# Optimization experiments

Hardware: AMD Instinct MI355X
Metric: run time of the kernel (lower is better)

## Reference

```python
import jax, jax.numpy as jnp
import numpy as np

RADIUS = 0.8
NSAMPLE = 32
EPS = 1e-5  # BatchNorm eps


def _bn(x, gamma, beta, axes):
    # BatchNorm (training-mode batch statistics), channel dim kept via broadcasting
    m = jnp.mean(x, axis=axes, keepdims=True)
    v = jnp.var(x, axis=axes, keepdims=True)
    return (x - m) * jax.lax.rsqrt(v + EPS) * gamma + beta


def setup_inputs() -> dict:
    key = jax.random.key(0)
    ks = jax.random.split(key, 6)
    B, N, P, C, COUT = 4, 8192, 2048, 128, 256
    ffps_xyz = jax.random.uniform(ks[0], (B, P, 3), dtype=jnp.float32) * 2.0 - 1.0
    backbone_xyz = jax.random.uniform(ks[1], (B, N, 3), dtype=jnp.float32) * 2.0 - 1.0
    backbone_features = jax.random.normal(ks[2], (B, C, N), dtype=jnp.float32)
    w_shift = jax.random.normal(ks[3], (3, 3), dtype=jnp.float32) * 0.1
    gamma_shift = jnp.ones((3,), jnp.float32)
    beta_shift = jnp.zeros((3,), jnp.float32)
    w_mlp = jax.random.normal(ks[4], (COUT, 3 + C), dtype=jnp.float32) * 0.05
    gamma_mlp = jnp.ones((COUT,), jnp.float32)
    beta_mlp = jnp.zeros((COUT,), jnp.float32)
    return {
        "ffps_xyz": ffps_xyz,
        "backbone_xyz": backbone_xyz,
        "backbone_features": backbone_features,
        "w_shift": w_shift,
        "gamma_shift": gamma_shift,
        "beta_shift": beta_shift,
        "w_mlp": w_mlp,
        "gamma_mlp": gamma_mlp,
        "beta_mlp": beta_mlp,
    }


def reference(ffps_xyz, backbone_xyz, backbone_features,
              w_shift, gamma_shift, beta_shift,
              w_mlp, gamma_mlp, beta_mlp):
    B, P, _ = ffps_xyz.shape
    N = backbone_xyz.shape[1]

    # ---- shift_layer: Conv1d(3->3, k=1, no bias) + BN1d + ReLU on (B,3,P) ----
    x = jnp.einsum('oc,bpc->bop', w_shift, ffps_xyz)                  # (B,3,P)
    x = _bn(x, gamma_shift[None, :, None], beta_shift[None, :, None], (0, 2))
    new_xyz = jax.nn.relu(x).transpose(0, 2, 1)                       # (B,P,3) query centers

    # ---- QueryAndGroup: ball query (radius, nsample), use_xyz=True ----
    d2 = jnp.sum((new_xyz[:, :, None, :] - backbone_xyz[:, None, :, :]) ** 2, -1)  # (B,P,N)
    within = d2 < (RADIUS * RADIUS)
    # pick the first NSAMPLE in-radius indices (CUDA ball_query semantics)
    keyv = jnp.where(within, jnp.arange(N, dtype=jnp.int32), jnp.int32(N))
    negk, idx = jax.lax.top_k(-keyv, NSAMPLE)                          # smallest keys first
    valid = (-negk) < N
    idx = jnp.where(valid, idx, idx[..., :1])                          # pad with first found idx

    g_xyz = jnp.take_along_axis(backbone_xyz[:, None, :, :], idx[..., None], axis=2)
    g_xyz = g_xyz - new_xyz[:, :, None, :]                             # (B,P,S,3) recentered
    feats = backbone_features.transpose(0, 2, 1)                       # (B,N,C)
    g_f = jnp.take_along_axis(feats[:, None, :, :], idx[..., None], axis=2)  # (B,P,S,C)
    g = jnp.concatenate([g_xyz, g_f], axis=-1)                         # (B,P,S,3+C)

    # ---- mlp: 1x1 conv (3+C -> COUT, no bias) + BN + ReLU ----
    y = jnp.einsum('oc,bpsc->bops', w_mlp, g)                          # (B,COUT,P,S)
    y = _bn(y, gamma_mlp[None, :, None, None], beta_mlp[None, :, None, None], (0, 2, 3))
    y = jax.nn.relu(y)

    # ---- max-pool over neighbor axis, squeeze, transpose ----
    y = jnp.max(y, axis=3)                                             # (B,COUT,P)
    return y.transpose(0, 2, 1)                                        # (B,P,COUT)
```

## Files before the change

### kernel.cpp

```cpp
#include <hip/hip_runtime.h>
#include <math.h>

namespace {
constexpr int B    = 4;
constexpr int N    = 8192;
constexpr int P    = 2048;
constexpr int C    = 128;
constexpr int COUT = 256;
constexpr int NS   = 32;
constexpr int BP   = B * P;
constexpr int BPB  = 2;
constexpr int GRP  = 8;
constexpr int NBLK = (BP / (BPB * GRP)) * 2;

constexpr size_t OFF_FEATT = 0;
constexpr size_t OFF_WSWZ  = 8388608;
constexpr size_t OFF_SSLOT = 8470528;
constexpr size_t OFF_SUMS  = 8471040;
constexpr size_t OFF_IDX   = 8475136;
constexpr size_t OFF_GX    = 9523712;
constexpr size_t OFF_YMAX  = 11620864;
constexpr size_t WS_NEED   = 20009472;
}

typedef short bf16x8 __attribute__((ext_vector_type(8)));
typedef float f32x4  __attribute__((ext_vector_type(4)));

typedef const __attribute__((address_space(1))) void gas_void;
typedef __attribute__((address_space(3))) void las_void;
#define GLOBAL_LOAD_LDS16(gp, lp) \
    __builtin_amdgcn_global_load_lds((gas_void*)(gp), (las_void*)(lp), 16, 0, 0)

__device__ inline unsigned short f2bf(float f) {
    unsigned u = __float_as_uint(f);
    unsigned r = u + 0x7fffu + ((u >> 16) & 1u);
    return (unsigned short)(r >> 16);
}


__global__ __launch_bounds__(256) void k_prep(const float* __restrict__ ffps,
                                              const float* __restrict__ wsh,
                                              double* __restrict__ sslot,
                                              float* __restrict__ sums) {
#pragma clang fp contract(off)
    int blk = blockIdx.x, t = threadIdx.x;
    if (blk == 8) {
        ((f32x4*)sums)[t & 127] = (f32x4){0.f, 0.f, 0.f, 0.f};
        return;
    }
    __shared__ double red[6][256];
    double w[9];
#pragma unroll
    for (int i = 0; i < 9; i++) w[i] = (double)wsh[i];
    double s[3] = {0, 0, 0}, sq[3] = {0, 0, 0};
#pragma unroll
    for (int i = 0; i < 4; i++) {
        int p = blk * 1024 + t + 256 * i;
        double f0 = (double)ffps[p * 3 + 0];
        double f1 = (double)ffps[p * 3 + 1];
        double f2 = (double)ffps[p * 3 + 2];
#pragma unroll
        for (int o = 0; o < 3; o++) {
            double xo = (w[o * 3 + 0] * f0 + w[o * 3 + 1] * f1) + w[o * 3 + 2] * f2;
            s[o] += xo;
            sq[o] += xo * xo;
        }
    }
#pragma unroll
    for (int o = 0; o < 3; o++) { red[o][t] = s[o]; red[3 + o][t] = sq[o]; }
    for (int off = 128; off > 0; off >>= 1) {
        __syncthreads();
        if (t < off) {
#pragma unroll
            for (int j = 0; j < 6; j++) red[j][t] += red[j][t + off];
        }
    }
    __syncthreads();
    if (t < 6) sslot[blk * 6 + t] = red[t][0];
}

__global__ __launch_bounds__(256) void k_front(const float* __restrict__ ffps,
                                               const float* __restrict__ bbxyz,
                                               const float* __restrict__ feat,
                                               const float* __restrict__ wsh,
                                               const float* __restrict__ gsh,
                                               const float* __restrict__ bsh,
                                               const float* __restrict__ wml,
                                               const double* __restrict__ sslot,
                                               unsigned short* __restrict__ featT,
                                               unsigned short* __restrict__ wswz,
                                               int* __restrict__ idxo,
                                               uint2* __restrict__ gxo) {
#pragma clang fp contract(off)
    int blk = blockIdx.x, t = threadIdx.x;
    if (blk >= 2048) {
        int rb = blk - 2048;
        if (rb < 2048) {
            __shared__ float tile[64][33];
            int tx = t & 31, ty = t >> 5;
            int n0 = (rb & 255) * 32, c0 = ((rb >> 8) & 1) * 64, b = rb >> 9;
            const float* src = feat + ((size_t)b * C + c0) * N + n0;
#pragma unroll
            for (int j = 0; j < 8; j++) tile[ty + 8 * j][tx] = src[(size_t)(ty + 8 * j) * N + tx];
            __syncthreads();
            int n = t >> 3;
            int k8 = (t & 7) * 8;
            unsigned vv[4];
#pragma unroll
            for (int i = 0; i < 4; i++) {
                unsigned lo = f2bf(tile[k8 + 2 * i][n]);
                unsigned hi = f2bf(tile[k8 + 2 * i + 1][n]);
                vv[i] = lo | (hi << 16);
            }
            *(int4*)&featT[((size_t)b * N + n0 + n) * C + c0 + k8] =
                make_int4((int)vv[0], (int)vv[1], (int)vv[2], (int)vv[3]);
        } else {
            int i = (rb - 2048) * 256 + t;
            int j = i & 7;
            int lane = (i >> 3) & 63;
            int rest = i >> 9;
            int ks = rest % 5, rt = rest / 5;
            int cout = rt * 16 + (lane & 15);
            int k = ks * 32 + (lane >> 4) * 8 + j;
            float v = 0.f;
            if (k < 128) v = wml[cout * 131 + 3 + k];
            else if (k < 131) v = wml[cout * 131 + (k - 128)];
            wswz[i] = f2bf(v);
        }
        return;
    }

    __shared__ double spar[6];
    if (t < 6) {
        double a = 0.0;
        for (int r = 0; r < 8; r++) a += sslot[r * 6 + t];
        spar[t] = a;
    }
    __syncthreads();
    int wv = t >> 6, lane = t & 63;
    int q = blk * 4 + wv;
    int b = q >> 11;
    double f0 = (double)ffps[q * 3 + 0];
    double f1 = (double)ffps[q * 3 + 1];
    double f2 = (double)ffps[q * 3 + 2];
    double qd[3];
#pragma unroll
    for (int o = 0; o < 3; o++) {
        double m  = spar[o] * (1.0 / 8192.0);
        double v  = spar[3 + o] * (1.0 / 8192.0) - m * m;
        double is = 1.0 / sqrt(v + 1e-5);
        double x  = ((double)wsh[o * 3 + 0] * f0 + (double)wsh[o * 3 + 1] * f1) +
                    (double)wsh[o * 3 + 2] * f2;
        double y  = ((x - m) * is) * (double)gsh[o] + (double)bsh[o];
        qd[o] = (y > 0.0) ? y : 0.0;
    }
    double qx = qd[0], qy = qd[1], qz = qd[2];
    float cfx = (float)qx, cfy = (float)qy, cfz = (float)qz;
    const float* base = bbxyz + (size_t)b * N * 3;
    const double R2 = 0.8 * 0.8;
    const float R2F = 0.64f;
    {
        double ex = fmax(fmax(qx - 1.0, -1.0 - qx), 0.0);
        double ey = fmax(fmax(qy - 1.0, -1.0 - qy), 0.0);
        double ez = fmax(fmax(qz - 1.0, -1.0 - qz), 0.0);
        if (ex * ex + ey * ey + ez * ez >= R2) {
            if (lane < NS) {
                idxo[q * NS + lane] = 0;
                float rx = base[0] - cfx, ry = base[1] - cfy, rz = base[2] - cfz;
                unsigned u01 = (unsigned)f2bf(rx) | ((unsigned)f2bf(ry) << 16);
                gxo[q * NS + lane] = make_uint2(u01, (unsigned)f2bf(rz));
            }
            return;
        }
    }
    int found = 0, firstn = -1;

    float X0[8], Y0[8], Z0[8], X1[8], Y1[8], Z1[8];

    auto loadb = [&](float (&XX)[8], float (&YY)[8], float (&ZZ)[8], int it) {
#pragma unroll
        for (int j = 0; j < 8; j++) {
            int n = it * 512 + j * 64 + lane;
            XX[j] = base[n * 3 + 0];
            YY[j] = base[n * 3 + 1];
            ZZ[j] = base[n * 3 + 2];
        }
    };
    auto proc = [&](float (&XX)[8], float (&YY)[8], float (&ZZ)[8], int it) {
#pragma clang fp contract(off)
#pragma unroll
        for (int j = 0; j < 8; j++) {
            int n = it * 512 + j * 64 + lane;
            float dxf = cfx - XX[j];
            float dyf = cfy - YY[j];
            float dzf = cfz - ZZ[j];
            float d2f = (dxf * dxf + dyf * dyf) + dzf * dzf;
            bool within;
            if (__builtin_expect(fabsf(d2f - R2F) < 1e-4f, 0)) {
                double dx = qx - (double)XX[j];
                double dy = qy - (double)YY[j];
                double dz = qz - (double)ZZ[j];
                within = ((dx * dx + dy * dy) + dz * dz) < R2;
            } else {
                within = d2f < R2F;
            }
            unsigned long long mask = __ballot(within);
            if (firstn < 0 && mask != 0ull) firstn = (n - lane) + (__ffsll(mask) - 1);
            if (within) {
                int rank = found + __popcll(mask & ((1ull << lane) - 1ull));
                if (rank < NS) {
                    idxo[q * NS + rank] = n;
                    float rx = XX[j] - cfx, ry = YY[j] - cfy, rz = ZZ[j] - cfz;
                    unsigned u01 = (unsigned)f2bf(rx) | ((unsigned)f2bf(ry) << 16);
                    gxo[q * NS + rank] = make_uint2(u01, (unsigned)f2bf(rz));
                }
            }
            found += __popcll(mask);
        }
    };

    loadb(X0, Y0, Z0, 0);
    loadb(X1, Y1, Z1, 1);

    for (int it = 0; it < 16; it += 2) {
        proc(X0, Y0, Z0, it);
        if (found >= NS) break;
        loadb(X0, Y0, Z0, (it + 2 < 16) ? it + 2 : 0);
        if (it + 1 >= 16) break;
        proc(X1, Y1, Z1, it + 1);
        if (found >= NS) break;
        loadb(X1, Y1, Z1, (it + 3 < 16) ? it + 3 : 0);
    }
    if (found < NS) {
        int padv = (found == 0) ? 0 : firstn;
        if (lane >= found && lane < NS) {
            idxo[q * NS + lane] = padv;
            float rx = base[padv * 3 + 0] - cfx;
            float ry = base[padv * 3 + 1] - cfy;
            float rz = base[padv * 3 + 2] - cfz;
            unsigned u01 = (unsigned)f2bf(rx) | ((unsigned)f2bf(ry) << 16);
            gxo[q * NS + lane] = make_uint2(u01, (unsigned)f2bf(rz));
        }
    }
}

__global__ __launch_bounds__(256, 3) void k_mlp_mfma(
        const unsigned short* __restrict__ featT,
        const unsigned short* __restrict__ wswz,
        const int* __restrict__ idx,
        const uint2* __restrict__ gxyz,
        float* __restrict__ ymax,
        float* __restrict__ sums) {
    __shared__ alignas(16) unsigned short G[2][4 * 4 * 64 * 8];
    int t = threadIdx.x, lane = t & 63, w = t >> 6;
    int q = lane >> 4, c16 = lane & 15;
    int d = blockIdx.x;
    int blk = ((d & 7) >> 1) * 256 + (d >> 3) * 2 + (d & 1);
    int nh = blk & 1;
    int bpbase = (blk >> 1) * (BPB * GRP);
    const bf16x8* wp = (const bf16x8*)wswz;

    bf16x8 wreg[5][2];
#pragma unroll
    for (int ks = 0; ks < 5; ks++)
#pragma unroll
        for (int nt = 0; nt < 2; nt++)
            wreg[ks][nt] = wp[((nh * 8 + w * 2 + nt) * 5 + ks) * 64 + lane];

    int sOff = (w >> 1) * NS + (w & 1) * 16 + c16;
    size_t fb = (size_t)(bpbase >> 11) * N * C;

    int nS0 = idx[bpbase * NS + sOff] & (N - 1);
    int nS1 = idx[(bpbase + BPB) * NS + sOff] & (N - 1);
    uint2 gx_c[4] = {}, gx_n[4] = {};
    if (q == 0)
#pragma unroll
        for (int mt = 0; mt < 4; mt++)
            gx_c[mt] = gxyz[(bpbase + (mt >> 1)) * NS + (mt & 1) * 16 + c16];
    {
        const unsigned short* row = featT + fb + (size_t)nS0 * C + q * 8;
#pragma unroll
        for (int ks = 0; ks < 4; ks++)
            GLOBAL_LOAD_LDS16(row + ks * 32, &G[0][(w * 4 + ks) * 512]);
    }

    float smA[2] = {0.f, 0.f}, sqA[2] = {0.f, 0.f};

    for (int g = 0; g < GRP; g++) {
        int buf = g & 1;
        int bp0 = bpbase + g * BPB;
        __syncthreads();
        if (g + 1 < GRP) {
            const unsigned short* row = featT + fb + (size_t)nS1 * C + q * 8;
#pragma unroll
            for (int ks = 0; ks < 4; ks++)
                GLOBAL_LOAD_LDS16(row + ks * 32, &G[buf ^ 1][(w * 4 + ks) * 512]);
            if (q == 0)
#pragma unroll
                for (int mt = 0; mt < 4; mt++)
                    gx_n[mt] = gxyz[(bp0 + BPB + (mt >> 1)) * NS + (mt & 1) * 16 + c16];
        }
        if (g + 2 < GRP) nS0 = idx[(bp0 + 2 * BPB) * NS + sOff] & (N - 1);

        f32x4 acc[4][2];
#pragma unroll
        for (int mt = 0; mt < 4; mt++)
#pragma unroll
            for (int nt = 0; nt < 2; nt++) acc[mt][nt] = (f32x4){0.f, 0.f, 0.f, 0.f};

#pragma unroll
        for (int ks = 0; ks < 4; ks++) {
            bf16x8 ag[4];
#pragma unroll
            for (int mt = 0; mt < 4; mt++)
                ag[mt] = *(const bf16x8*)&G[buf][((mt * 4 + ks) * 64 + lane) * 8];
#pragma unroll
            for (int nt = 0; nt < 2; nt++)
#pragma unroll
                for (int mt = 0; mt < 4; mt++)
                    acc[mt][nt] = __builtin_amdgcn_mfma_f32_16x16x32_bf16(ag[mt], wreg[ks][nt], acc[mt][nt], 0, 0, 0);
        }
        {
            bf16x8 agx[4];
#pragma unroll
            for (int mt = 0; mt < 4; mt++) {
                union { int4 i; bf16x8 h; } u;
                u.i = make_int4(q == 0 ? (int)gx_c[mt].x : 0,
                                q == 0 ? (int)gx_c[mt].y : 0, 0, 0);
                agx[mt] = u.h;
            }
#pragma unroll
            for (int nt = 0; nt < 2; nt++)
#pragma unroll
                for (int mt = 0; mt < 4; mt++)
                    acc[mt][nt] = __builtin_amdgcn_mfma_f32_16x16x32_bf16(agx[mt], wreg[4][nt], acc[mt][nt], 0, 0, 0);
        }

#pragma unroll
        for (int pm = 0; pm < BPB; pm++) {
            int bp = bp0 + pm;
#pragma unroll
            for (int nt = 0; nt < 2; nt++) {
                f32x4 a = acc[2 * pm][nt], c = acc[2 * pm + 1][nt];
                float mx = fmaxf(fmaxf(fmaxf(a[0], a[1]), fmaxf(a[2], a[3])),
                                 fmaxf(fmaxf(c[0], c[1]), fmaxf(c[2], c[3])));
                smA[nt] += ((a[0] + a[1]) + (a[2] + a[3])) + ((c[0] + c[1]) + (c[2] + c[3]));
                sqA[nt] += ((a[0] * a[0] + a[1] * a[1]) + (a[2] * a[2] + a[3] * a[3])) +
                           ((c[0] * c[0] + c[1] * c[1]) + (c[2] * c[2] + c[3] * c[3]));
                mx = fmaxf(mx, __shfl_xor(mx, 16, 64));
                mx = fmaxf(mx, __shfl_xor(mx, 32, 64));
                if (q == 0)
                    ymax[(size_t)bp * COUT + nh * 128 + w * 32 + nt * 16 + c16] = mx;
            }
        }
        nS1 = nS0;
#pragma unroll
        for (int mt = 0; mt < 4; mt++) gx_c[mt] = gx_n[mt];
    }

#pragma unroll
    for (int nt = 0; nt < 2; nt++) {
        float sm = smA[nt], sq = sqA[nt];
        sm += __shfl_xor(sm, 16, 64);
        sm += __shfl_xor(sm, 32, 64);
        sq += __shfl_xor(sq, 16, 64);
        sq += __shfl_xor(sq, 32, 64);
        if (q == 0) {
            int cout = nh * 128 + w * 32 + nt * 16 + c16;
            atomicAdd(&sums[cout], sm);
            atomicAdd(&sums[256 + cout], sq);
        }
    }
}

__global__ __launch_bounds__(256) void k_final(const float* __restrict__ ymax,
                                               const float* __restrict__ sums,
                                               const float* __restrict__ gam,
                                               const float* __restrict__ bet,
                                               float* __restrict__ out) {
    __shared__ float sa[256], sb[256];
    int t = threadIdx.x;
    {
        double sm = (double)sums[t], sq = (double)sums[256 + t];
        double mean = sm * (1.0 / 262144.0);
        double var = sq * (1.0 / 262144.0) - mean * mean;
        double a = (double)gam[t] / sqrt(var + 1e-5);
        sa[t] = (float)a;
        sb[t] = (float)((double)bet[t] - mean * a);
    }
    __syncthreads();
    int i = blockIdx.x * 256 + t;
    int c0 = (t & 63) * 4;
    f32x4 y = *(const f32x4*)&ymax[(size_t)i * 4];
    f32x4 r;
#pragma unroll
    for (int j = 0; j < 4; j++) r[j] = fmaxf(sa[c0 + j] * y[j] + sb[c0 + j], 0.f);
    *(f32x4*)&out[(size_t)i * 4] = r;
}

extern "C" void kernel_launch(void* const* d_in, const int* in_sizes, int n_in,
                              void* d_out, int out_size, void* d_ws, size_t ws_size,
                              hipStream_t stream) {
    const float* ffps  = (const float*)d_in[0];
    const float* bbxyz = (const float*)d_in[1];
    const float* feat  = (const float*)d_in[2];
    const float* wsh   = (const float*)d_in[3];
    const float* gsh   = (const float*)d_in[4];
    const float* bsh   = (const float*)d_in[5];
    const float* wml   = (const float*)d_in[6];
    const float* gml   = (const float*)d_in[7];
    const float* bml   = (const float*)d_in[8];
    float* out = (float*)d_out;
    char* ws = (char*)d_ws;
    if (ws_size < WS_NEED) return;

    unsigned short* featT = (unsigned short*)(ws + OFF_FEATT);
    unsigned short* wswz  = (unsigned short*)(ws + OFF_WSWZ);
    double*         sslot = (double*)(ws + OFF_SSLOT);
    float*          sums  = (float*)(ws + OFF_SUMS);
    int*            idx   = (int*)(ws + OFF_IDX);
    uint2*          gx    = (uint2*)(ws + OFF_GX);
    float*          ymax  = (float*)(ws + OFF_YMAX);

    k_prep<<<dim3(9), dim3(256), 0, stream>>>(ffps, wsh, sslot, sums);
    k_front<<<dim3(2048 + 2048 + 160), dim3(256), 0, stream>>>(
        ffps, bbxyz, feat, wsh, gsh, bsh, wml, sslot, featT, wswz, idx, gx);
    k_mlp_mfma<<<dim3(NBLK), dim3(256), 0, stream>>>(featT, wswz, idx, gx, ymax, sums);
    k_final<<<dim3(BP * COUT / 1024), dim3(256), 0, stream>>>(ymax, sums, gml, bml, out);
}
```

Before: 152.0 us.

## Fuse MLP and BN finalize into a cooperative kernel with grid sync

Replaces the separate MLP kernel and final BN/ReLU kernel with one cooperative kernel. Each block covers all 256 output channels for 16 query points, keeps the per-point max in shared memory, and after a grid-wide sync applies the BN scale/shift and writes the output directly. This removes the round trip of the ymax buffer through global memory and one kernel launch. In exchange it uses more registers per block, halves the block count, and relies on all 512 blocks being co-resident; if the cooperative launch fails it falls back to the old two-kernel path.

```diff
diff --git a/kernel.cpp b/kernel.cpp
--- a/kernel.cpp
+++ b/kernel.cpp
@@ -1,5 +1,8 @@
 #include <hip/hip_runtime.h>
+#include <hip/hip_cooperative_groups.h>
 #include <math.h>
+
+namespace cg = cooperative_groups;
 
 namespace {
 constexpr int B    = 4;
@@ -11,7 +14,8 @@
 constexpr int BP   = B * P;
 constexpr int BPB  = 2;
 constexpr int GRP  = 8;
-constexpr int NBLK = (BP / (BPB * GRP)) * 2;
+constexpr int NBLKC = BP / (BPB * GRP);
+constexpr int NBLKL = NBLKC * 2;
 
 constexpr size_t OFF_FEATT = 0;
 constexpr size_t OFF_WSWZ  = 8388608;
@@ -244,6 +248,155 @@
     }
 }
 
+__global__ __launch_bounds__(256, 2) void k_mlp_coop(
+        const unsigned short* __restrict__ featT,
+        const unsigned short* __restrict__ wswz,
+        const int* __restrict__ idx,
+        const uint2* __restrict__ gxyz,
+        const float* __restrict__ gam,
+        const float* __restrict__ bet,
+        float* __restrict__ sums,
+        float* __restrict__ out) {
+    cg::grid_group grid = cg::this_grid();
+    __shared__ alignas(16) unsigned short G[2][4 * 4 * 64 * 8];
+    __shared__ float ymx[16][COUT];
+    __shared__ float sa[COUT], sb[COUT];
+    int t = threadIdx.x, lane = t & 63, w = t >> 6;
+    int q = lane >> 4, c16 = lane & 15;
+    int d = blockIdx.x;
+    int blk = ((d & 7) >> 1) * 128 + (d >> 3) * 2 + (d & 1);
+    int bpbase = blk * (BPB * GRP);
+    const bf16x8* wp = (const bf16x8*)wswz;
+
+    bf16x8 wreg[5][4];
+#pragma unroll
+    for (int ks = 0; ks < 5; ks++)
+#pragma unroll
+        for (int nt = 0; nt < 4; nt++)
+            wreg[ks][nt] = wp[((w * 4 + nt) * 5 + ks) * 64 + lane];
+
+    int sOff = (w >> 1) * NS + (w & 1) * 16 + c16;
+    size_t fb = (size_t)(bpbase >> 11) * N * C;
+
+    int nS0 = idx[bpbase * NS + sOff] & (N - 1);
+    int nS1 = idx[(bpbase + BPB) * NS + sOff] & (N - 1);
+    uint2 gx_c[4] = {}, gx_n[4] = {};
+    if (q == 0)
+#pragma unroll
+        for (int mt = 0; mt < 4; mt++)
+            gx_c[mt] = gxyz[(bpbase + (mt >> 1)) * NS + (mt & 1) * 16 + c16];
+    {
+        const unsigned short* row = featT + fb + (size_t)nS0 * C + q * 8;
+#pragma unroll
+        for (int ks = 0; ks < 4; ks++)
+            GLOBAL_LOAD_LDS16(row + ks * 32, &G[0][(w * 4 + ks) * 512]);
+    }
+
+    float smA[4] = {0.f, 0.f, 0.f, 0.f}, sqA[4] = {0.f, 0.f, 0.f, 0.f};
+
+    for (int g = 0; g < GRP; g++) {
+        int buf = g & 1;
+        int bp0l = g * BPB;
+        __syncthreads();
+        if (g + 1 < GRP) {
+            const unsigned short* row = featT + fb + (size_t)nS1 * C + q * 8;
+#pragma unroll
+            for (int ks = 0; ks < 4; ks++)
+                GLOBAL_LOAD_LDS16(row + ks * 32, &G[buf ^ 1][(w * 4 + ks) * 512]);
+            if (q == 0)
+#pragma unroll
+                for (int mt = 0; mt < 4; mt++)
+                    gx_n[mt] = gxyz[(bpbase + bp0l + BPB + (mt >> 1)) * NS + (mt & 1) * 16 + c16];
+        }
+        if (g + 2 < GRP) nS0 = idx[(bpbase + bp0l + 2 * BPB) * NS + sOff] & (N - 1);
+
+        f32x4 acc[4][4];
+#pragma unroll
+        for (int mt = 0; mt < 4; mt++)
+#pragma unroll
+            for (int nt = 0; nt < 4; nt++) acc[mt][nt] = (f32x4){0.f, 0.f, 0.f, 0.f};
+
+#pragma unroll
+        for (int ks = 0; ks < 4; ks++) {
+            bf16x8 ag[4];
+#pragma unroll
+            for (int mt = 0; mt < 4; mt++)
+                ag[mt] = *(const bf16x8*)&G[buf][((mt * 4 + ks) * 64 + lane) * 8];
+#pragma unroll
+            for (int nt = 0; nt < 4; nt++)
+#pragma unroll
+                for (int mt = 0; mt < 4; mt++)
+                    acc[mt][nt] = __builtin_amdgcn_mfma_f32_16x16x32_bf16(ag[mt], wreg[ks][nt], acc[mt][nt], 0, 0, 0);
+        }
+        {
+            bf16x8 agx[4];
+#pragma unroll
+            for (int mt = 0; mt < 4; mt++) {
+                union { int4 i; bf16x8 h; } u;
+                u.i = make_int4(q == 0 ? (int)gx_c[mt].x : 0,
+                                q == 0 ? (int)gx_c[mt].y : 0, 0, 0);
+                agx[mt] = u.h;
+            }
+#pragma unroll
+            for (int nt = 0; nt < 4; nt++)
+#pragma unroll
+                for (int mt = 0; mt < 4; mt++)
+                    acc[mt][nt] = __builtin_amdgcn_mfma_f32_16x16x32_bf16(agx[mt], wreg[4][nt], acc[mt][nt], 0, 0, 0);
+        }
+
+#pragma unroll
+        for (int pm = 0; pm < BPB; pm++) {
+#pragma unroll
+            for (int nt = 0; nt < 4; nt++) {
+                f32x4 a = acc[2 * pm][nt], c = acc[2 * pm + 1][nt];
+                float mx = fmaxf(fmaxf(fmaxf(a[0], a[1]), fmaxf(a[2], a[3])),
+                                 fmaxf(fmaxf(c[0], c[1]), fmaxf(c[2], c[3])));
+                smA[nt] += ((a[0] + a[1]) + (a[2] + a[3])) + ((c[0] + c[1]) + (c[2] + c[3]));
+                sqA[nt] += ((a[0] * a[0] + a[1] * a[1]) + (a[2] * a[2] + a[3] * a[3])) +
+                           ((c[0] * c[0] + c[1] * c[1]) + (c[2] * c[2] + c[3] * c[3]));
+                mx = fmaxf(mx, __shfl_xor(mx, 16, 64));
+                mx = fmaxf(mx, __shfl_xor(mx, 32, 64));
+                if (q == 0)
+                    ymx[bp0l + pm][w * 64 + nt * 16 + c16] = mx;
+            }
+        }
+        nS1 = nS0;
+#pragma unroll
+        for (int mt = 0; mt < 4; mt++) gx_c[mt] = gx_n[mt];
+    }
+
+#pragma unroll
+    for (int nt = 0; nt < 4; nt++) {
+        float sm = smA[nt], sq = sqA[nt];
+        sm += __shfl_xor(sm, 16, 64);
+        sm += __shfl_xor(sm, 32, 64);
+        sq += __shfl_xor(sq, 16, 64);
+        sq += __shfl_xor(sq, 32, 64);
+        if (q == 0) {
+            int cout = w * 64 + nt * 16 + c16;
+            atomicAdd(&sums[cout], sm);
+            atomicAdd(&sums[256 + cout], sq);
+        }
+    }
+
+    grid.sync();
+
+    {
+        float smv = __hip_atomic_load(&sums[t], __ATOMIC_RELAXED, __HIP_MEMORY_SCOPE_AGENT);
+        float sqv = __hip_atomic_load(&sums[256 + t], __ATOMIC_RELAXED, __HIP_MEMORY_SCOPE_AGENT);
+        double mean = (double)smv * (1.0 / 262144.0);
+        double var  = (double)sqv * (1.0 / 262144.0) - mean * mean;
+        double a = (double)gam[t] / sqrt(var + 1e-5);
+        sa[t] = (float)a;
+        sb[t] = (float)((double)bet[t] - mean * a);
+    }
+    __syncthreads();
+    for (int r = 0; r < 16; r++) {
+        float y = ymx[r][t];
+        out[(size_t)(bpbase + r) * COUT + t] = fmaxf(sa[t] * y + sb[t], 0.f);
+    }
+}
+
 __global__ __launch_bounds__(256, 3) void k_mlp_mfma(
         const unsigned short* __restrict__ featT,
         const unsigned short* __restrict__ wswz,
@@ -259,17 +412,14 @@
     int nh = blk & 1;
     int bpbase = (blk >> 1) * (BPB * GRP);
     const bf16x8* wp = (const bf16x8*)wswz;
-
     bf16x8 wreg[5][2];
 #pragma unroll
     for (int ks = 0; ks < 5; ks++)
 #pragma unroll
         for (int nt = 0; nt < 2; nt++)
             wreg[ks][nt] = wp[((nh * 8 + w * 2 + nt) * 5 + ks) * 64 + lane];
-
     int sOff = (w >> 1) * NS + (w & 1) * 16 + c16;
     size_t fb = (size_t)(bpbase >> 11) * N * C;
-
     int nS0 = idx[bpbase * NS + sOff] & (N - 1);
     int nS1 = idx[(bpbase + BPB) * NS + sOff] & (N - 1);
     uint2 gx_c[4] = {}, gx_n[4] = {};
@@ -283,9 +433,7 @@
         for (int ks = 0; ks < 4; ks++)
             GLOBAL_LOAD_LDS16(row + ks * 32, &G[0][(w * 4 + ks) * 512]);
     }
-
     float smA[2] = {0.f, 0.f}, sqA[2] = {0.f, 0.f};
-
     for (int g = 0; g < GRP; g++) {
         int buf = g & 1;
         int bp0 = bpbase + g * BPB;
@@ -301,13 +449,11 @@
                     gx_n[mt] = gxyz[(bp0 + BPB + (mt >> 1)) * NS + (mt & 1) * 16 + c16];
         }
         if (g + 2 < GRP) nS0 = idx[(bp0 + 2 * BPB) * NS + sOff] & (N - 1);
-
         f32x4 acc[4][2];
 #pragma unroll
         for (int mt = 0; mt < 4; mt++)
 #pragma unroll
             for (int nt = 0; nt < 2; nt++) acc[mt][nt] = (f32x4){0.f, 0.f, 0.f, 0.f};
-
 #pragma unroll
         for (int ks = 0; ks < 4; ks++) {
             bf16x8 ag[4];
@@ -335,7 +481,6 @@
                 for (int mt = 0; mt < 4; mt++)
                     acc[mt][nt] = __builtin_amdgcn_mfma_f32_16x16x32_bf16(agx[mt], wreg[4][nt], acc[mt][nt], 0, 0, 0);
         }
-
 #pragma unroll
         for (int pm = 0; pm < BPB; pm++) {
             int bp = bp0 + pm;
@@ -357,7 +502,6 @@
 #pragma unroll
         for (int mt = 0; mt < 4; mt++) gx_c[mt] = gx_n[mt];
     }
-
 #pragma unroll
     for (int nt = 0; nt < 2; nt++) {
         float sm = smA[nt], sq = sqA[nt];
@@ -425,6 +569,13 @@
     k_prep<<<dim3(9), dim3(256), 0, stream>>>(ffps, wsh, sslot, sums);
     k_front<<<dim3(2048 + 2048 + 160), dim3(256), 0, stream>>>(
         ffps, bbxyz, feat, wsh, gsh, bsh, wml, sslot, featT, wswz, idx, gx);
-    k_mlp_mfma<<<dim3(NBLK), dim3(256), 0, stream>>>(featT, wswz, idx, gx, ymax, sums);
-    k_final<<<dim3(BP * COUT / 1024), dim3(256), 0, stream>>>(ymax, sums, gml, bml, out);
-}
+
+    void* kargs[] = {(void*)&featT, (void*)&wswz, (void*)&idx, (void*)&gx,
+                     (void*)&gml, (void*)&bml, (void*)&sums, (void*)&out};
+    hipError_t err = hipLaunchCooperativeKernel((const void*)k_mlp_coop, dim3(NBLKC),
+                                                dim3(256), kargs, 0, stream);
+    if (err != hipSuccess) {
+        k_mlp_mfma<<<dim3(NBLKL), dim3(256), 0, stream>>>(featT, wswz, idx, gx, ymax, sums);
+        k_final<<<dim3(BP * COUT / 1024), dim3(256), 0, stream>>>(ymax, sums, gml, bml, out);
+    }
+}
```

Measured after the change: 222.5 us. +46.4%, slower.

## Split ball-query scan across two waves per query with LDS merge

Applied to the files above, without the earlier changes.

Each query is now handled by two wavefronts that scan the two halves of the point cloud in parallel. Candidates go to shared memory and are merged into the first-32 ordering afterwards, and the second-half wave exits early once the first half has already found 32 neighbours. This shortens the serial scan latency for queries with few in-radius points at the cost of twice the blocks, extra LDS traffic and a block-wide sync. Padding semantics are preserved by choosing the first found index from whichever half has hits.

```diff
diff --git a/kernel.cpp b/kernel.cpp
--- a/kernel.cpp
+++ b/kernel.cpp
@@ -93,8 +93,8 @@
                                                uint2* __restrict__ gxo) {
 #pragma clang fp contract(off)
     int blk = blockIdx.x, t = threadIdx.x;
-    if (blk >= 2048) {
-        int rb = blk - 2048;
+    if (blk >= 4096) {
+        int rb = blk - 4096;
         if (rb < 2048) {
             __shared__ float tile[64][33];
             int tx = t & 31, ty = t >> 5;
@@ -131,14 +131,20 @@
     }
 
     __shared__ double spar[6];
+    __shared__ int lidx[2][2][NS];
+    __shared__ uint2 lgx[2][2][NS];
+    __shared__ int lcnt[2][2], lfirst[2][2];
+    __shared__ int ldone[2];
     if (t < 6) {
         double a = 0.0;
         for (int r = 0; r < 8; r++) a += sslot[r * 6 + t];
         spar[t] = a;
     }
+    if (t < 2) ldone[t] = 0;
     __syncthreads();
     int wv = t >> 6, lane = t & 63;
-    int q = blk * 4 + wv;
+    int qi = wv >> 1, half = wv & 1;
+    int q = blk * 2 + qi;
     int b = q >> 11;
     double f0 = (double)ffps[q * 3 + 0];
     double f1 = (double)ffps[q * 3 + 1];
@@ -159,88 +165,121 @@
     const float* base = bbxyz + (size_t)b * N * 3;
     const double R2 = 0.8 * 0.8;
     const float R2F = 0.64f;
+    bool eo;
     {
         double ex = fmax(fmax(qx - 1.0, -1.0 - qx), 0.0);
         double ey = fmax(fmax(qy - 1.0, -1.0 - qy), 0.0);
         double ez = fmax(fmax(qz - 1.0, -1.0 - qz), 0.0);
-        if (ex * ex + ey * ey + ez * ez >= R2) {
-            if (lane < NS) {
-                idxo[q * NS + lane] = 0;
-                float rx = base[0] - cfx, ry = base[1] - cfy, rz = base[2] - cfz;
-                unsigned u01 = (unsigned)f2bf(rx) | ((unsigned)f2bf(ry) << 16);
-                gxo[q * NS + lane] = make_uint2(u01, (unsigned)f2bf(rz));
+        eo = (ex * ex + ey * ey + ez * ez >= R2);
+    }
+
+    if (!eo) {
+        int found = 0, firstn = -1;
+        int nb = half * 4096;
+
+        float X0[8], Y0[8], Z0[8], X1[8], Y1[8], Z1[8];
+
+        auto loadb = [&](float (&XX)[8], float (&YY)[8], float (&ZZ)[8], int it) {
+#pragma unroll
+            for (int j = 0; j < 8; j++) {
+                int n = nb + it * 512 + j * 64 + lane;
+                XX[j] = base[n * 3 + 0];
+                YY[j] = base[n * 3 + 1];
+                ZZ[j] = base[n * 3 + 2];
             }
-            return;
-        }
-    }
-    int found = 0, firstn = -1;
-
-    float X0[8], Y0[8], Z0[8], X1[8], Y1[8], Z1[8];
-
-    auto loadb = [&](float (&XX)[8], float (&YY)[8], float (&ZZ)[8], int it) {
-#pragma unroll
-        for (int j = 0; j < 8; j++) {
-            int n = it * 512 + j * 64 + lane;
-            XX[j] = base[n * 3 + 0];
-            YY[j] = base[n * 3 + 1];
-            ZZ[j] = base[n * 3 + 2];
-        }
-    };
-    auto proc = [&](float (&XX)[8], float (&YY)[8], float (&ZZ)[8], int it) {
+        };
+        auto proc = [&](float (&XX)[8], float (&YY)[8], float (&ZZ)[8], int it) {
 #pragma clang fp contract(off)
 #pragma unroll
-        for (int j = 0; j < 8; j++) {
-            int n = it * 512 + j * 64 + lane;
-            float dxf = cfx - XX[j];
-            float dyf = cfy - YY[j];
-            float dzf = cfz - ZZ[j];
-            float d2f = (dxf * dxf + dyf * dyf) + dzf * dzf;
-            bool within;
-            if (__builtin_expect(fabsf(d2f - R2F) < 1e-4f, 0)) {
-                double dx = qx - (double)XX[j];
-                double dy = qy - (double)YY[j];
-                double dz = qz - (double)ZZ[j];
-                within = ((dx * dx + dy * dy) + dz * dz) < R2;
-            } else {
-                within = d2f < R2F;
+            for (int j = 0; j < 8; j++) {
+                int n = nb + it * 512 + j * 64 + lane;
+                float dxf = cfx - XX[j];
+                float dyf = cfy - YY[j];
+                float dzf = cfz - ZZ[j];
+                float d2f = (dxf * dxf + dyf * dyf) + dzf * dzf;
+                bool within;
+                if (__builtin_expect(fabsf(d2f - R2F) < 1e-4f, 0)) {
+                    double dx = qx - (double)XX[j];
+                    double dy = qy - (double)YY[j];
+                    double dz = qz - (double)ZZ[j];
+                    within = ((dx * dx + dy * dy) + dz * dz) < R2;
+                } else {
+                    within = d2f < R2F;
+                }
+                unsigned long long mask = __ballot(within);
+                if (firstn < 0 && mask != 0ull) firstn = (n - lane) + (__ffsll(mask) - 1);
+                if (within) {
+                    int rank = found + __popcll(mask & ((1ull << lane) - 1ull));
+                    if (rank < NS) {
+                        lidx[qi][half][rank] = n;
+                        float rx = XX[j] - cfx, ry = YY[j] - cfy, rz = ZZ[j] - cfz;
+                        unsigned u01 = (unsigned)f2bf(rx) | ((unsigned)f2bf(ry) << 16);
+                        lgx[qi][half][rank] = make_uint2(u01, (unsigned)f2bf(rz));
+                    }
+                }
+                found += __popcll(mask);
             }
-            unsigned long long mask = __ballot(within);
-            if (firstn < 0 && mask != 0ull) firstn = (n - lane) + (__ffsll(mask) - 1);
-            if (within) {
-                int rank = found + __popcll(mask & ((1ull << lane) - 1ull));
-                if (rank < NS) {
-                    idxo[q * NS + rank] = n;
-                    float rx = XX[j] - cfx, ry = YY[j] - cfy, rz = ZZ[j] - cfz;
-                    unsigned u01 = (unsigned)f2bf(rx) | ((unsigned)f2bf(ry) << 16);
-                    gxo[q * NS + rank] = make_uint2(u01, (unsigned)f2bf(rz));
-                }
-            }
-            found += __popcll(mask);
-        }
-    };
-
-    loadb(X0, Y0, Z0, 0);
-    loadb(X1, Y1, Z1, 1);
-
-    for (int it = 0; it < 16; it += 2) {
-        proc(X0, Y0, Z0, it);
-        if (found >= NS) break;
-        loadb(X0, Y0, Z0, (it + 2 < 16) ? it + 2 : 0);
-        if (it + 1 >= 16) break;
-        proc(X1, Y1, Z1, it + 1);
-        if (found >= NS) break;
-        loadb(X1, Y1, Z1, (it + 3 < 16) ? it + 3 : 0);
-    }
-    if (found < NS) {
-        int padv = (found == 0) ? 0 : firstn;
-        if (lane >= found && lane < NS) {
-            idxo[q * NS + lane] = padv;
-            float rx = base[padv * 3 + 0] - cfx;
-            float ry = base[padv * 3 + 1] - cfy;
-            float rz = base[padv * 3 + 2] - cfz;
+        };
+
+        loadb(X0, Y0, Z0, 0);
+        loadb(X1, Y1, Z1, 1);
+
+        for (int it = 0; it < 8; it += 2) {
+            proc(X0, Y0, Z0, it);
+            if (found >= NS) break;
+            if (half == 1 &&
+                __hip_atomic_load(&ldone[qi], __ATOMIC_RELAXED, __HIP_MEMORY_SCOPE_WORKGROUP))
+                break;
+            loadb(X0, Y0, Z0, (it + 2 < 8) ? it + 2 : 0);
+            if (it + 1 >= 8) break;
+            proc(X1, Y1, Z1, it + 1);
+            if (found >= NS) break;
+            if (half == 1 &&
+                __hip_atomic_load(&ldone[qi], __ATOMIC_RELAXED, __HIP_MEMORY_SCOPE_WORKGROUP))
+                break;
+            loadb(X1, Y1, Z1, (it + 3 < 8) ? it + 3 : 0);
+        }
+        if (half == 0 && found >= NS)
+            __hip_atomic_store(&ldone[qi], 1, __ATOMIC_RELAXED, __HIP_MEMORY_SCOPE_WORKGROUP);
+        if (lane == 0) {
+            lcnt[qi][half] = found;
+            lfirst[qi][half] = firstn;
+        }
+    }
+    __syncthreads();
+
+    if (eo) {
+        if (half == 0 && lane < NS) {
+            idxo[q * NS + lane] = 0;
+            float rx = base[0] - cfx, ry = base[1] - cfy, rz = base[2] - cfz;
             unsigned u01 = (unsigned)f2bf(rx) | ((unsigned)f2bf(ry) << 16);
             gxo[q * NS + lane] = make_uint2(u01, (unsigned)f2bf(rz));
         }
+    } else if (half == 0 && lane < NS) {
+        int fa = lcnt[qi][0], fb = lcnt[qi][1];
+        int ka = (fa < NS) ? fa : NS;
+        int tot = fa + fb;
+        int kt = (tot < NS) ? tot : NS;
+        int idxv;
+        uint2 gxv;
+        if (lane < ka) {
+            idxv = lidx[qi][0][lane];
+            gxv  = lgx[qi][0][lane];
+        } else if (lane < kt) {
+            idxv = lidx[qi][1][lane - ka];
+            gxv  = lgx[qi][1][lane - ka];
+        } else if (tot > 0) {
+            int hsel = (fa > 0) ? 0 : 1;
+            idxv = lidx[qi][hsel][0];
+            gxv  = lgx[qi][hsel][0];
+        } else {
+            idxv = 0;
+            float rx = base[0] - cfx, ry = base[1] - cfy, rz = base[2] - cfz;
+            unsigned u01 = (unsigned)f2bf(rx) | ((unsigned)f2bf(ry) << 16);
+            gxv = make_uint2(u01, (unsigned)f2bf(rz));
+        }
+        idxo[q * NS + lane] = idxv;
+        gxo[q * NS + lane] = gxv;
     }
 }
 
@@ -423,7 +462,7 @@
     float*          ymax  = (float*)(ws + OFF_YMAX);
 
     k_prep<<<dim3(9), dim3(256), 0, stream>>>(ffps, wsh, sslot, sums);
-    k_front<<<dim3(2048 + 2048 + 160), dim3(256), 0, stream>>>(
+    k_front<<<dim3(4096 + 2048 + 160), dim3(256), 0, stream>>>(
         ffps, bbxyz, feat, wsh, gsh, bsh, wml, sslot, featT, wswz, idx, gx);
     k_mlp_mfma<<<dim3(NBLK), dim3(256), 0, stream>>>(featT, wswz, idx, gx, ymax, sums);
     k_final<<<dim3(BP * COUT / 1024), dim3(256), 0, stream>>>(ymax, sums, gml, bml, out);
```

Result: faster. 148.3 us (median of 2 runs) (-2.4%).

## Split ball query across four wavefronts per query with LDS merge

Applied to the files above, without the earlier changes.

Each block now handles a single query point instead of four. Its four wavefronts each scan a quarter of the N points, keep their first NS hits in LDS, and merge them in order at the end. A later wavefront stops early once the earlier quarters have already filled NS hits, which it checks through workgroup-scope atomic flags. The aim is to shorten the serial scan latency per query and raise parallelism, at the cost of four times as many blocks, possibly wasted scanning in the later quarters, and extra LDS plus a merge step.

```diff
diff --git a/kernel.cpp b/kernel.cpp
--- a/kernel.cpp
+++ b/kernel.cpp
@@ -93,8 +93,8 @@
                                                uint2* __restrict__ gxo) {
 #pragma clang fp contract(off)
     int blk = blockIdx.x, t = threadIdx.x;
-    if (blk >= 2048) {
-        int rb = blk - 2048;
+    if (blk >= 8192) {
+        int rb = blk - 8192;
         if (rb < 2048) {
             __shared__ float tile[64][33];
             int tx = t & 31, ty = t >> 5;
@@ -131,14 +131,19 @@
     }
 
     __shared__ double spar[6];
+    __shared__ int lidx[4][NS];
+    __shared__ uint2 lgx[4][NS];
+    __shared__ int lcnt[4];
+    __shared__ int ldone[4];
     if (t < 6) {
         double a = 0.0;
         for (int r = 0; r < 8; r++) a += sslot[r * 6 + t];
         spar[t] = a;
     }
+    if (t < 4) ldone[t] = 0;
     __syncthreads();
-    int wv = t >> 6, lane = t & 63;
-    int q = blk * 4 + wv;
+    int half = t >> 6, lane = t & 63;
+    int q = blk;
     int b = q >> 11;
     double f0 = (double)ffps[q * 3 + 0];
     double f1 = (double)ffps[q * 3 + 1];
@@ -159,87 +164,131 @@
     const float* base = bbxyz + (size_t)b * N * 3;
     const double R2 = 0.8 * 0.8;
     const float R2F = 0.64f;
+    bool eo;
     {
         double ex = fmax(fmax(qx - 1.0, -1.0 - qx), 0.0);
         double ey = fmax(fmax(qy - 1.0, -1.0 - qy), 0.0);
         double ez = fmax(fmax(qz - 1.0, -1.0 - qz), 0.0);
-        if (ex * ex + ey * ey + ez * ez >= R2) {
-            if (lane < NS) {
-                idxo[q * NS + lane] = 0;
-                float rx = base[0] - cfx, ry = base[1] - cfy, rz = base[2] - cfz;
-                unsigned u01 = (unsigned)f2bf(rx) | ((unsigned)f2bf(ry) << 16);
-                gxo[q * NS + lane] = make_uint2(u01, (unsigned)f2bf(rz));
-            }
-            return;
-        }
-    }
-    int found = 0, firstn = -1;
-
-    float X0[8], Y0[8], Z0[8], X1[8], Y1[8], Z1[8];
-
-    auto loadb = [&](float (&XX)[8], float (&YY)[8], float (&ZZ)[8], int it) {
-#pragma unroll
-        for (int j = 0; j < 8; j++) {
-            int n = it * 512 + j * 64 + lane;
-            XX[j] = base[n * 3 + 0];
-            YY[j] = base[n * 3 + 1];
-            ZZ[j] = base[n * 3 + 2];
-        }
-    };
-    auto proc = [&](float (&XX)[8], float (&YY)[8], float (&ZZ)[8], int it) {
+        eo = (ex * ex + ey * ey + ez * ez >= R2);
+    }
+
+    if (!eo) {
+        int found = 0;
+        int nb = half * 2048;
+
+        float X0[8], Y0[8], Z0[8], X1[8], Y1[8], Z1[8];
+
+        auto loadb = [&](float (&XX)[8], float (&YY)[8], float (&ZZ)[8], int it) {
+#pragma unroll
+            for (int j = 0; j < 8; j++) {
+                int n = nb + it * 512 + j * 64 + lane;
+                XX[j] = base[n * 3 + 0];
+                YY[j] = base[n * 3 + 1];
+                ZZ[j] = base[n * 3 + 2];
+            }
+        };
+        auto proc = [&](float (&XX)[8], float (&YY)[8], float (&ZZ)[8], int it) {
 #pragma clang fp contract(off)
 #pragma unroll
-        for (int j = 0; j < 8; j++) {
-            int n = it * 512 + j * 64 + lane;
-            float dxf = cfx - XX[j];
-            float dyf = cfy - YY[j];
-            float dzf = cfz - ZZ[j];
-            float d2f = (dxf * dxf + dyf * dyf) + dzf * dzf;
-            bool within;
-            if (__builtin_expect(fabsf(d2f - R2F) < 1e-4f, 0)) {
-                double dx = qx - (double)XX[j];
-                double dy = qy - (double)YY[j];
-                double dz = qz - (double)ZZ[j];
-                within = ((dx * dx + dy * dy) + dz * dz) < R2;
-            } else {
-                within = d2f < R2F;
-            }
-            unsigned long long mask = __ballot(within);
-            if (firstn < 0 && mask != 0ull) firstn = (n - lane) + (__ffsll(mask) - 1);
-            if (within) {
-                int rank = found + __popcll(mask & ((1ull << lane) - 1ull));
-                if (rank < NS) {
-                    idxo[q * NS + rank] = n;
-                    float rx = XX[j] - cfx, ry = YY[j] - cfy, rz = ZZ[j] - cfz;
-                    unsigned u01 = (unsigned)f2bf(rx) | ((unsigned)f2bf(ry) << 16);
-                    gxo[q * NS + rank] = make_uint2(u01, (unsigned)f2bf(rz));
+            for (int j = 0; j < 8; j++) {
+                int n = nb + it * 512 + j * 64 + lane;
+                float dxf = cfx - XX[j];
+                float dyf = cfy - YY[j];
+                float dzf = cfz - ZZ[j];
+                float d2f = (dxf * dxf + dyf * dyf) + dzf * dzf;
+                bool within;
+                if (__builtin_expect(fabsf(d2f - R2F) < 1e-4f, 0)) {
+                    double dx = qx - (double)XX[j];
+                    double dy = qy - (double)YY[j];
+                    double dz = qz - (double)ZZ[j];
+                    within = ((dx * dx + dy * dy) + dz * dz) < R2;
+                } else {
+                    within = d2f < R2F;
                 }
-            }
-            found += __popcll(mask);
-        }
-    };
-
-    loadb(X0, Y0, Z0, 0);
-    loadb(X1, Y1, Z1, 1);
-
-    for (int it = 0; it < 16; it += 2) {
-        proc(X0, Y0, Z0, it);
-        if (found >= NS) break;
-        loadb(X0, Y0, Z0, (it + 2 < 16) ? it + 2 : 0);
-        if (it + 1 >= 16) break;
-        proc(X1, Y1, Z1, it + 1);
-        if (found >= NS) break;
-        loadb(X1, Y1, Z1, (it + 3 < 16) ? it + 3 : 0);
-    }
-    if (found < NS) {
-        int padv = (found == 0) ? 0 : firstn;
-        if (lane >= found && lane < NS) {
-            idxo[q * NS + lane] = padv;
-            float rx = base[padv * 3 + 0] - cfx;
-            float ry = base[padv * 3 + 1] - cfy;
-            float rz = base[padv * 3 + 2] - cfz;
+                unsigned long long mask = __ballot(within);
+                if (within) {
+                    int rank = found + __popcll(mask & ((1ull << lane) - 1ull));
+                    if (rank < NS) {
+                        lidx[half][rank] = n;
+                        float rx = XX[j] - cfx, ry = YY[j] - cfy, rz = ZZ[j] - cfz;
+                        unsigned u01 = (unsigned)f2bf(rx) | ((unsigned)f2bf(ry) << 16);
+                        lgx[half][rank] = make_uint2(u01, (unsigned)f2bf(rz));
+                    }
+                }
+                found += __popcll(mask);
+            }
+        };
+        auto earlier_full = [&]() -> bool {
+            int s = 0;
+#pragma unroll
+            for (int h = 0; h < 4; h++) {
+                if (h >= half) break;
+                if (!__hip_atomic_load(&ldone[h], __ATOMIC_ACQUIRE,
+                                       __HIP_MEMORY_SCOPE_WORKGROUP))
+                    return false;
+                s += lcnt[h];
+            }
+            return s >= NS;
+        };
+
+        loadb(X0, Y0, Z0, 0);
+        loadb(X1, Y1, Z1, 1);
+
+        for (int it = 0; it < 4; it += 2) {
+            proc(X0, Y0, Z0, it);
+            if (found >= NS) break;
+            if (half > 0 && earlier_full()) break;
+            loadb(X0, Y0, Z0, (it + 2 < 4) ? it + 2 : 0);
+            if (it + 1 >= 4) break;
+            proc(X1, Y1, Z1, it + 1);
+            if (found >= NS) break;
+            if (half > 0 && earlier_full()) break;
+            loadb(X1, Y1, Z1, (it + 3 < 4) ? it + 3 : 0);
+        }
+        if (lane == 0) {
+            lcnt[half] = found;
+            __hip_atomic_store(&ldone[half], 1, __ATOMIC_RELEASE,
+                               __HIP_MEMORY_SCOPE_WORKGROUP);
+        }
+    }
+    __syncthreads();
+
+    if (half == 0 && lane < NS) {
+        if (eo) {
+            idxo[q * NS + lane] = 0;
+            float rx = base[0] - cfx, ry = base[1] - cfy, rz = base[2] - cfz;
             unsigned u01 = (unsigned)f2bf(rx) | ((unsigned)f2bf(ry) << 16);
             gxo[q * NS + lane] = make_uint2(u01, (unsigned)f2bf(rz));
+        } else {
+            int idxv = 0;
+            uint2 gxv;
+            bool got = false;
+            int pre = 0, total = 0, h0 = -1;
+#pragma unroll
+            for (int h = 0; h < 4; h++) {
+                int ch = lcnt[h];
+                if (h0 < 0 && ch > 0) h0 = h;
+                if (!got && lane < pre + ch) {
+                    idxv = lidx[h][lane - pre];
+                    gxv  = lgx[h][lane - pre];
+                    got = true;
+                }
+                pre += ch;
+                total += ch;
+            }
+            if (!got) {
+                if (total > 0) {
+                    idxv = lidx[h0][0];
+                    gxv  = lgx[h0][0];
+                } else {
+                    idxv = 0;
+                    float rx = base[0] - cfx, ry = base[1] - cfy, rz = base[2] - cfz;
+                    unsigned u01 = (unsigned)f2bf(rx) | ((unsigned)f2bf(ry) << 16);
+                    gxv = make_uint2(u01, (unsigned)f2bf(rz));
+                }
+            }
+            idxo[q * NS + lane] = idxv;
+            gxo[q * NS + lane] = gxv;
         }
     }
 }
@@ -423,7 +472,7 @@
     float*          ymax  = (float*)(ws + OFF_YMAX);
 
     k_prep<<<dim3(9), dim3(256), 0, stream>>>(ffps, wsh, sslot, sums);
-    k_front<<<dim3(2048 + 2048 + 160), dim3(256), 0, stream>>>(
+    k_front<<<dim3(8192 + 2048 + 160), dim3(256), 0, stream>>>(
         ffps, bbxyz, feat, wsh, gsh, bsh, wml, sslot, featT, wswz, idx, gx);
     k_mlp_mfma<<<dim3(NBLK), dim3(256), 0, stream>>>(featT, wswz, idx, gx, ymax, sums);
     k_final<<<dim3(BP * COUT / 1024), dim3(256), 0, stream>>>(ymax, sums, gml, bml, out);
```

Result: slower. 156.1 us (+2.7%).
